# Performance work log

Measured on AMD Instinct MI355X. Metric: run time of the kernel, lower is better.

Reference implementation:

```python
import jax, jax.numpy as jnp
import numpy as np

B, N, EPG = 64, 512, 8192
E = B * EPG
K1 = int(np.ceil(0.8 * N))    # 410
K2 = int(np.ceil(0.8 * K1))   # 328


def setup_inputs() -> dict:
    key = jax.random.key(0)
    ks = jax.random.split(key, 32)
    x = jax.random.normal(ks[0], (B * N, 32), jnp.float32)
    edge_attr = jax.random.normal(ks[1], (E, 100), jnp.float32)
    src_l = jax.random.randint(ks[2], (E,), 0, N)
    dst_l = jax.random.randint(ks[3], (E,), 0, N)
    off = jnp.repeat(jnp.arange(B, dtype=jnp.int64) * N, EPG)
    edge_index = jnp.stack([src_l + off, dst_l + off]).astype(jnp.int64)
    batch = jnp.repeat(jnp.arange(B, dtype=jnp.int64), N)

    def lin(k, fin, fout):
        s = 1.0 / np.sqrt(fin)
        k1, k2 = jax.random.split(k)
        return (jax.random.uniform(k1, (fin, fout), jnp.float32, -s, s),
                jax.random.uniform(k2, (fout,), jnp.float32, -s, s))

    dec1_w, dec1_b = lin(ks[4], 100, 64)
    dec2_w, dec2_b = lin(ks[5], 64, 32)
    mlp1_w, mlp1_b = lin(ks[6], 32, 128)
    mlp2_w, mlp2_b = lin(ks[7], 128, 256)
    pool1_w = jax.random.normal(ks[8], (256,), jnp.float32) * 0.1
    gat_w = jax.random.normal(ks[9], (256, 256), jnp.float32) * (1.0 / np.sqrt(256))
    gat_att_src = jax.random.normal(ks[10], (4, 64), jnp.float32) * 0.1
    gat_att_dst = jax.random.normal(ks[11], (4, 64), jnp.float32) * 0.1
    gat_b = jnp.zeros((256,), jnp.float32)
    pool2_w = jax.random.normal(ks[12], (256,), jnp.float32) * 0.1
    lin1_w, lin1_b = lin(ks[13], 512, 128)
    lin2_w, lin2_b = lin(ks[14], 128, 64)
    lin3_w, lin3_b = lin(ks[15], 64, 2)
    return dict(x=x, edge_index=edge_index, batch=batch, edge_attr=edge_attr,
                dec1_w=dec1_w, dec1_b=dec1_b, dec2_w=dec2_w, dec2_b=dec2_b,
                mlp1_w=mlp1_w, mlp1_b=mlp1_b, mlp2_w=mlp2_w, mlp2_b=mlp2_b,
                pool1_w=pool1_w, gat_w=gat_w, gat_att_src=gat_att_src,
                gat_att_dst=gat_att_dst, gat_b=gat_b, pool2_w=pool2_w,
                lin1_w=lin1_w, lin1_b=lin1_b, lin2_w=lin2_w, lin2_b=lin2_b,
                lin3_w=lin3_w, lin3_b=lin3_b)


def _forward(x, edge_attr, dec1_w, dec1_b, dec2_w, dec2_b, mlp1_w, mlp1_b,
             mlp2_w, mlp2_b, pool1_w, gat_w, gat_att_src, gat_att_dst, gat_b,
             pool2_w, lin1_w, lin1_b, lin2_w, lin2_b, lin3_w, lin3_b,
             src, dst):
    # edge encoder
    ea = jax.nn.relu(edge_attr @ dec1_w + dec1_b)
    ea = jax.nn.relu(ea @ dec2_w + dec2_b)                       # [E,32]
    # GINEConv (eps=0): sum_j relu(x_j + e_ji), then mlp((1+eps)x + aggr)
    msg = jax.nn.relu(x[src] + ea)
    agg = jax.ops.segment_sum(msg, dst, num_segments=B * N)
    h = x + agg
    h = jax.nn.relu(h @ mlp1_w + mlp1_b) @ mlp2_w + mlp2_b       # [BN,256]
    h = jax.nn.relu(h)
    # TopKPooling 1 (uniform graphs -> fixed k)
    s = jnp.tanh((h @ pool1_w) / jnp.linalg.norm(pool1_w))       # [BN]
    topv, topi = jax.lax.top_k(s.reshape(B, N), K1)              # [B,K1]
    gperm = (topi + jnp.arange(B)[:, None] * N).reshape(-1)
    hp = h[gperm] * topv.reshape(-1)[:, None]                    # [B*K1,256]
    kept = jnp.zeros(B * N, bool).at[gperm].set(True)
    newid = jnp.zeros(B * N, jnp.int32).at[gperm].set(jnp.arange(B * K1, dtype=jnp.int32))
    src1, dst1 = newid[src], newid[dst]
    valid = kept[src] & kept[dst]
    # readout 1: global max + mean pool
    hr = hp.reshape(B, K1, 256)
    x1 = jnp.concatenate([hr.max(axis=1), hr.mean(axis=1)], axis=-1)  # [B,512]
    # GATConv(256, 64, heads=4) with self-loops; invalid edges masked
    Nk = B * K1
    loops = jnp.arange(Nk, dtype=jnp.int32)
    src2 = jnp.concatenate([src1, loops])
    dst2 = jnp.concatenate([dst1, loops])
    valid2 = jnp.concatenate([valid, jnp.ones(Nk, bool)])
    xl = (hp @ gat_w).reshape(Nk, 4, 64)
    a_src = (xl * gat_att_src).sum(-1)                           # [Nk,4]
    a_dst = (xl * gat_att_dst).sum(-1)
    logit = jax.nn.leaky_relu(a_src[src2] + a_dst[dst2], 0.2)    # [E2,4]
    logit = jnp.where(valid2[:, None], logit, -jnp.inf)
    m = jax.ops.segment_max(logit, dst2, num_segments=Nk)
    e = jnp.where(valid2[:, None], jnp.exp(logit - m[dst2]), 0.0)
    den = jax.ops.segment_sum(e, dst2, num_segments=Nk)
    alpha = e / den[dst2]
    out = jax.ops.segment_sum(alpha[:, :, None] * xl[src2], dst2, num_segments=Nk)
    g = jax.nn.relu(out.reshape(Nk, 256) + gat_b)
    # TopKPooling 2 (pooled edges unused downstream)
    s2 = jnp.tanh((g @ pool2_w) / jnp.linalg.norm(pool2_w))
    topv2, topi2 = jax.lax.top_k(s2.reshape(B, K1), K2)
    gperm2 = (topi2 + jnp.arange(B)[:, None] * K1).reshape(-1)
    gp = (g[gperm2] * topv2.reshape(-1)[:, None]).reshape(B, K2, 256)
    x2 = jnp.concatenate([gp.max(axis=1), gp.mean(axis=1)], axis=-1)
    # head (dropout = identity in eval)
    z = x1 + x2
    z = jax.nn.relu(z @ lin1_w + lin1_b)
    z = jax.nn.relu(z @ lin2_w + lin2_b)
    return jax.nn.log_softmax(z @ lin3_w + lin3_b, axis=-1)     # [B,2]


def reference(x, edge_index, batch, edge_attr, dec1_w, dec1_b, dec2_w, dec2_b,
              mlp1_w, mlp1_b, mlp2_w, mlp2_b, pool1_w, gat_w, gat_att_src,
              gat_att_dst, gat_b, pool2_w, lin1_w, lin1_b, lin2_w, lin2_b,
              lin3_w, lin3_b):
    src = edge_index[0].astype(jnp.int32)
    dst = edge_index[1].astype(jnp.int32)
    return _forward(x, edge_attr, dec1_w, dec1_b, dec2_w, dec2_b, mlp1_w,
                    mlp1_b, mlp2_w, mlp2_b, pool1_w, gat_w, gat_att_src,
                    gat_att_dst, gat_b, pool2_w, lin1_w, lin1_b, lin2_w,
                    lin2_b, lin3_w, lin3_b, src, dst)
```

## Files before the change

kernel.cpp:

```cpp
#include <hip/hip_runtime.h>
#include <math.h>

#define B_   64
#define N_   512
#define E_   524288
#define BN_  32768
#define K1_  410
#define K2_  328
#define NK_  26240
#define KC_  25

__device__ __forceinline__ float lrelu(float x) { return x > 0.f ? x : 0.2f * x; }

__global__ __launch_bounds__(256) void norm_kernel(const float* __restrict__ p1,
                                                   const float* __restrict__ p2,
                                                   float* __restrict__ norms) {
    __shared__ float r1[256], r2[256];
    int t = threadIdx.x;
    float a = p1[t], b = p2[t];
    r1[t] = a * a; r2[t] = b * b;
    for (int o = 128; o > 0; o >>= 1) {
        __syncthreads();
        if (t < o) { r1[t] += r1[t + o]; r2[t] += r2[t + o]; }
    }
    __syncthreads();
    if (t == 0) { norms[0] = sqrtf(r1[0]); norms[1] = sqrtf(r2[0]); }
}

template <int NSEG>
__global__ __launch_bounds__(1024) void scan_kernel(int* __restrict__ cnt, int* __restrict__ offsets)
{
    __shared__ int part[1024];
    int t = threadIdx.x;
    const int CH = (NSEG + 1023) / 1024;
    int base = t * CH;
    int sum = 0;
    for (int i = 0; i < CH; ++i) { int gi = base + i; if (gi < NSEG) sum += cnt[gi]; }
    part[t] = sum;
    __syncthreads();
    for (int o = 1; o < 1024; o <<= 1) {
        int v = (t >= o) ? part[t - o] : 0;
        __syncthreads();
        part[t] += v;
        __syncthreads();
    }
    int run = (t == 0) ? 0 : part[t - 1];
    for (int i = 0; i < CH; ++i) {
        int gi = base + i;
        if (gi < NSEG) { offsets[gi] = run; run += cnt[gi]; cnt[gi] = 0; }
    }
    if (t == 1023) offsets[NSEG] = part[1023];
}

__global__ __launch_bounds__(256) void count_node_kernel(const int* __restrict__ dstG,
                                                         int* __restrict__ cnt_node)
{
    int e = blockIdx.x * blockDim.x + threadIdx.x;
    atomicAdd(&cnt_node[dstG[e]], 1);
}

__global__ __launch_bounds__(256) void fill_node_kernel(const int* __restrict__ dstG,
                                                        const int* __restrict__ offs_node,
                                                        int* __restrict__ cnt_node,
                                                        int* __restrict__ pos_e)
{
    int e = blockIdx.x * blockDim.x + threadIdx.x;
    int d = dstG[e];
    int p = offs_node[d] + atomicAdd(&cnt_node[d], 1);
    pos_e[e] = p;
}

__global__ __launch_bounds__(256) void edge_mlp_kernel(
    const float* __restrict__ edge_attr, const int* __restrict__ srcG,
    const int* __restrict__ pos_e,
    const float* __restrict__ x,
    const float* __restrict__ W1, const float* __restrict__ b1,
    const float* __restrict__ W2, const float* __restrict__ b2,
    float* __restrict__ msg_sorted)
{
    __shared__ float bufAT[KC_][68];
    __shared__ float w1cT[KC_][64];
    __shared__ float ea1T[64][68];
    __shared__ float w2s[64][32];
    __shared__ float b2s[32];
    __shared__ int   srcs[64], poss[64];

    int tid = threadIdx.x;
    int eb  = blockIdx.x * 64;

    if (tid < 64) { srcs[tid] = srcG[eb + tid]; poss[tid] = pos_e[eb + tid]; }
    for (int i = tid; i < 64 * 32; i += 256) w2s[i >> 5][i & 31] = W2[i];
    if (tid >= 192 && tid < 224) b2s[tid - 192] = b2[tid - 192];

    int tx = tid & 15, ty = tid >> 4;
    float b1v[4];
#pragma unroll
    for (int j = 0; j < 4; ++j) b1v[j] = b1[tx * 4 + j];

    float acc[4][4] = {};

    float raA[7], raB[7], rw[7];
    auto issueA = [&](int kc, float (&ra)[7]) {
#pragma unroll
        for (int u = 0; u < 7; ++u) {
            int i = tid + u * 256;
            if (i < 1600) {
                int e = i / 25, k = i - e * 25;
                ra[u] = edge_attr[(size_t)(eb + e) * 100 + kc + k];
            }
        }
    };
    auto issueW = [&](int kc) {
#pragma unroll
        for (int u = 0; u < 7; ++u) {
            int i = tid + u * 256;
            if (i < 1600) rw[u] = W1[(size_t)(kc + (i >> 6)) * 64 + (i & 63)];
        }
    };
    auto lwriteA = [&](float (&ra)[7]) {
#pragma unroll
        for (int u = 0; u < 7; ++u) {
            int i = tid + u * 256;
            if (i < 1600) {
                int e = i / 25, k = i - e * 25;
                bufAT[k][e] = ra[u];
            }
        }
    };
    auto lwriteW = [&]() {
#pragma unroll
        for (int u = 0; u < 7; ++u) {
            int i = tid + u * 256;
            if (i < 1600) w1cT[i >> 6][i & 63] = rw[u];
        }
    };

    issueA(0, raA);
    issueW(0);
    issueA(KC_, raB);
    lwriteA(raA); lwriteW();
    __syncthreads();

#pragma unroll
    for (int c = 0; c < 4; ++c) {
        if (c == 0) issueA(2 * KC_, raA);
        if (c == 1) issueA(3 * KC_, raB);
        if (c < 3)  issueW((c + 1) * KC_);
#pragma unroll 5
        for (int k = 0; k < KC_; ++k) {
            float4 a4 = *(const float4*)&bufAT[k][ty * 4];
            float4 w4 = *(const float4*)&w1cT[k][tx * 4];
            float a[4] = { a4.x, a4.y, a4.z, a4.w };
            float w[4] = { w4.x, w4.y, w4.z, w4.w };
#pragma unroll
            for (int i = 0; i < 4; ++i)
#pragma unroll
                for (int j = 0; j < 4; ++j) acc[i][j] += a[i] * w[j];
        }
        if (c < 3) {
            __syncthreads();
            if ((c & 1) == 0) lwriteA(raB);
            else              lwriteA(raA);
            lwriteW();
            __syncthreads();
        }
    }
#pragma unroll
    for (int j = 0; j < 4; ++j) {
        float4 v;
        v.x = fmaxf(acc[0][j] + b1v[j], 0.f);
        v.y = fmaxf(acc[1][j] + b1v[j], 0.f);
        v.z = fmaxf(acc[2][j] + b1v[j], 0.f);
        v.w = fmaxf(acc[3][j] + b1v[j], 0.f);
        *(float4*)&ea1T[tx * 4 + j][ty * 4] = v;
    }
    __syncthreads();

    int e0 = (tid >> 3) * 2;
    int c0 = (tid & 7) * 4;
    float acc2[2][4] = {};
    for (int k = 0; k < 64; ++k) {
        float2 a2 = *(const float2*)&ea1T[k][e0];
        float4 w4 = *(const float4*)&w2s[k][c0];
        float w[4] = { w4.x, w4.y, w4.z, w4.w };
#pragma unroll
        for (int j = 0; j < 4; ++j) {
            acc2[0][j] += a2.x * w[j]; acc2[1][j] += a2.y * w[j];
        }
    }
#pragma unroll
    for (int r = 0; r < 2; ++r) {
        int e = e0 + r, s = srcs[e];
        const float4 xv = *(const float4*)(x + (size_t)s * 32 + c0);
        float xa[4] = { xv.x, xv.y, xv.z, xv.w };
        float4 m;
        m.x = fmaxf(xa[0] + fmaxf(acc2[r][0] + b2s[c0 + 0], 0.f), 0.f);
        m.y = fmaxf(xa[1] + fmaxf(acc2[r][1] + b2s[c0 + 1], 0.f), 0.f);
        m.z = fmaxf(xa[2] + fmaxf(acc2[r][2] + b2s[c0 + 2], 0.f), 0.f);
        m.w = fmaxf(xa[3] + fmaxf(acc2[r][3] + b2s[c0 + 3], 0.f), 0.f);
        *(float4*)(msg_sorted + (size_t)poss[e] * 32 + c0) = m;
    }
}

__global__ __launch_bounds__(256) void segsum_kernel(const float* __restrict__ msg_sorted,
                                                     const int* __restrict__ offs_n,
                                                     float* __restrict__ agg)
{
    int wid  = (blockIdx.x * blockDim.x + threadIdx.x) >> 6;
    int lane = threadIdx.x & 63;
    if (wid >= BN_) return;
    int off0 = offs_n[wid], off1 = offs_n[wid + 1];
    int col = lane & 31, rr = lane >> 5;
    float sum = 0.f;
    for (int j = off0 + rr; j < off1; j += 2)
        sum += msg_sorted[(size_t)j * 32 + col];
    sum += __shfl_xor(sum, 32);
    if (lane < 32) agg[(size_t)wid * 32 + col] = sum;
}

template <int ACT, bool HASBIAS, bool HASA2>
__global__ __launch_bounds__(256) void gemm_tile128(
    const float* __restrict__ A, const float* __restrict__ A2,
    const float* __restrict__ W, const float* __restrict__ bias,
    float* __restrict__ C, int M, int N, int K)
{
    __shared__ float As[16][132];
    __shared__ float Ws[16][132];
    int tid = threadIdx.x;
    int tx = tid & 15, ty = tid >> 4;
    int mb = blockIdx.y * 128, nb = blockIdx.x * 128;
    float acc[8][8] = {};

    int am = tid & 127;
    int ak = (tid >> 7) * 8;
    int wk = tid >> 4;
    int wn = (tid & 15) * 8;

    for (int kt = 0; kt < K; kt += 16) {
        {
            const float* pa = A + (size_t)(mb + am) * K + kt + ak;
            float4 v0 = *(const float4*)(pa);
            float4 v1 = *(const float4*)(pa + 4);
            if (HASA2) {
                const float* pb = A2 + (size_t)(mb + am) * K + kt + ak;
                float4 u0 = *(const float4*)(pb);
                float4 u1 = *(const float4*)(pb + 4);
                v0.x += u0.x; v0.y += u0.y; v0.z += u0.z; v0.w += u0.w;
                v1.x += u1.x; v1.y += u1.y; v1.z += u1.z; v1.w += u1.w;
            }
            As[ak + 0][am] = v0.x; As[ak + 1][am] = v0.y;
            As[ak + 2][am] = v0.z; As[ak + 3][am] = v0.w;
            As[ak + 4][am] = v1.x; As[ak + 5][am] = v1.y;
            As[ak + 6][am] = v1.z; As[ak + 7][am] = v1.w;
        }
        {
            const float* pw = W + (size_t)(kt + wk) * N + nb + wn;
            *(float4*)&Ws[wk][wn]     = *(const float4*)(pw);
            *(float4*)&Ws[wk][wn + 4] = *(const float4*)(pw + 4);
        }
        __syncthreads();
#pragma unroll
        for (int k2 = 0; k2 < 16; ++k2) {
            float4 a0 = *(const float4*)&As[k2][ty * 8];
            float4 a1 = *(const float4*)&As[k2][ty * 8 + 4];
            float4 w0 = *(const float4*)&Ws[k2][tx * 4];
            float4 w1 = *(const float4*)&Ws[k2][64 + tx * 4];
            float a[8] = { a0.x, a0.y, a0.z, a0.w, a1.x, a1.y, a1.z, a1.w };
            float w[8] = { w0.x, w0.y, w0.z, w0.w, w1.x, w1.y, w1.z, w1.w };
#pragma unroll
            for (int i = 0; i < 8; ++i)
#pragma unroll
                for (int j = 0; j < 8; ++j) acc[i][j] += a[i] * w[j];
        }
        __syncthreads();
    }
#pragma unroll
    for (int i = 0; i < 8; ++i) {
        int m = mb + ty * 8 + i;
        int col0 = nb + tx * 4, col1 = nb + 64 + tx * 4;
        float r[8];
#pragma unroll
        for (int j = 0; j < 4; ++j) {
            float v = acc[i][j];
            if (HASBIAS) v += bias[col0 + j];
            if (ACT == 1) v = fmaxf(v, 0.f);
            r[j] = v;
        }
#pragma unroll
        for (int j = 4; j < 8; ++j) {
            float v = acc[i][j];
            if (HASBIAS) v += bias[col1 + j - 4];
            if (ACT == 1) v = fmaxf(v, 0.f);
            r[j] = v;
        }
        float4 o0 = { r[0], r[1], r[2], r[3] };
        float4 o1 = { r[4], r[5], r[6], r[7] };
        *(float4*)&C[(size_t)m * N + col0] = o0;
        *(float4*)&C[(size_t)m * N + col1] = o1;
    }
}

__global__ __launch_bounds__(256) void scores_kernel(const float* __restrict__ P,
                                                     const float* __restrict__ w,
                                                     const float* __restrict__ norms, int nidx,
                                                     float* __restrict__ s, int R)
{
    int wid  = (blockIdx.x * blockDim.x + threadIdx.x) >> 6;
    int lane = threadIdx.x & 63;
    if (wid >= R) return;
    float acc = 0.f;
#pragma unroll
    for (int r = 0; r < 4; ++r) {
        int d = r * 64 + lane;
        acc += P[(size_t)wid * 256 + d] * w[d];
    }
    for (int o = 32; o > 0; o >>= 1) acc += __shfl_xor(acc, o);
    if (lane == 0) s[wid] = tanhf(acc / norms[nidx]);
}

__device__ void bitonic_desc512(float* val, int* idx, int t) {
    for (int k = 2; k <= 512; k <<= 1) {
        for (int j = k >> 1; j > 0; j >>= 1) {
            __syncthreads();
            int ixj = t ^ j;
            if (ixj > t) {
                float v0 = val[t], v1 = val[ixj];
                int   i0 = idx[t], i1 = idx[ixj];
                bool before = (v0 > v1) || (v0 == v1 && i0 < i1);
                bool dir = ((t & k) == 0);
                bool doswap = dir ? (!before) : before;
                if (doswap) { val[t] = v1; val[ixj] = v0; idx[t] = i1; idx[ixj] = i0; }
            }
        }
    }
    __syncthreads();
}

__global__ __launch_bounds__(512) void topk1_kernel(const float* __restrict__ s,
                                                    float* __restrict__ topval,
                                                    int* __restrict__ topnode,
                                                    int* __restrict__ kept,
                                                    int* __restrict__ newid)
{
    __shared__ float val[512];
    __shared__ int   idx[512];
    int b = blockIdx.x, t = threadIdx.x;
    val[t] = s[b * N_ + t]; idx[t] = t;
    bitonic_desc512(val, idx, t);
    if (t < K1_) {
        int node = b * N_ + idx[t];
        int orow = b * K1_ + t;
        topnode[orow] = node;
        topval[orow]  = val[t];
        kept[node]  = 1;
        newid[node] = orow;
    }
}

__global__ __launch_bounds__(256) void gather_scale_kernel(const float* __restrict__ h,
                                                           const int* __restrict__ topnode,
                                                           const float* __restrict__ topval,
                                                           float* __restrict__ hp)
{
    int gid = blockIdx.x * blockDim.x + threadIdx.x;
    int row = gid >> 6, q = gid & 63;
    float4 v = *(const float4*)(h + (size_t)topnode[row] * 256 + q * 4);
    float tv = topval[row];
    float4 o; o.x = v.x * tv; o.y = v.y * tv; o.z = v.z * tv; o.w = v.w * tv;
    *(float4*)(hp + (size_t)row * 256 + q * 4) = o;
}

__global__ __launch_bounds__(1024) void readout1_kernel(const float* __restrict__ hp,
                                                        float* __restrict__ zbuf)
{
    __shared__ float rmx[1024], rsm[1024];
    int b = blockIdx.x >> 2, cg = blockIdx.x & 3;
    int tid = threadIdx.x;
    int cl = tid & 63, rg = tid >> 6;
    int c = cg * 64 + cl;
    float mx = -INFINITY, sm = 0.f;
    for (int j = rg; j < K1_; j += 16) {
        float v = hp[((size_t)b * K1_ + j) * 256 + c];
        mx = fmaxf(mx, v); sm += v;
    }
    rmx[tid] = mx; rsm[tid] = sm;
    __syncthreads();
    if (tid < 512) { rmx[tid] = fmaxf(rmx[tid], rmx[tid + 512]); rsm[tid] += rsm[tid + 512]; }
    __syncthreads();
    if (tid < 256) { rmx[tid] = fmaxf(rmx[tid], rmx[tid + 256]); rsm[tid] += rsm[tid + 256]; }
    __syncthreads();
    if (tid < 128) { rmx[tid] = fmaxf(rmx[tid], rmx[tid + 128]); rsm[tid] += rsm[tid + 128]; }
    __syncthreads();
    if (tid < 64) {
        zbuf[b * 512 + c]       = fmaxf(rmx[tid], rmx[tid + 64]);
        zbuf[b * 512 + 256 + c] = (rsm[tid] + rsm[tid + 64]) / (float)K1_;
    }
}

__global__ __launch_bounds__(256) void attcoef_kernel(const float* __restrict__ xl,
                                                      const float* __restrict__ att_src,
                                                      const float* __restrict__ att_dst,
                                                      float* __restrict__ a_src,
                                                      float* __restrict__ a_dst)
{
    int wid  = (blockIdx.x * blockDim.x + threadIdx.x) >> 6;
    int lane = threadIdx.x & 63;
    if (wid >= NK_) return;
    float vs[4], vd[4];
#pragma unroll
    for (int r = 0; r < 4; ++r) {
        int d = r * 64 + lane;
        float v = xl[(size_t)wid * 256 + d];
        vs[r] = v * att_src[d];
        vd[r] = v * att_dst[d];
    }
    for (int o = 32; o > 0; o >>= 1) {
#pragma unroll
        for (int r = 0; r < 4; ++r) {
            vs[r] += __shfl_xor(vs[r], o);
            vd[r] += __shfl_xor(vd[r], o);
        }
    }
    if (lane == 0) {
#pragma unroll
        for (int r = 0; r < 4; ++r) {
            a_src[wid * 4 + r] = vs[r];
            a_dst[wid * 4 + r] = vd[r];
        }
    }
}

__global__ __launch_bounds__(256) void count_kernel(const int* __restrict__ srcG,
                                                    const int* __restrict__ dstG,
                                                    const int* __restrict__ kept,
                                                    const int* __restrict__ newid,
                                                    int* __restrict__ cnt)
{
    int e = blockIdx.x * blockDim.x + threadIdx.x;
    int s = srcG[e], d = dstG[e];
    if (kept[s] && kept[d]) atomicAdd(&cnt[newid[d]], 1);
}

__global__ __launch_bounds__(256) void fill_kernel(const int* __restrict__ srcG,
                                                   const int* __restrict__ dstG,
                                                   const int* __restrict__ kept,
                                                   const int* __restrict__ newid,
                                                   const int* __restrict__ offsets,
                                                   int* __restrict__ cnt,
                                                   int* __restrict__ csr_src)
{
    int e = blockIdx.x * blockDim.x + threadIdx.x;
    int s = srcG[e], d = dstG[e];
    if (kept[s] && kept[d]) {
        int d1 = newid[d];
        int p = offsets[d1] + atomicAdd(&cnt[d1], 1);
        csr_src[p] = newid[s];
    }
}

__global__ __launch_bounds__(256) void gat_agg_kernel(const float* __restrict__ xl,
                                                      const float* __restrict__ a_src,
                                                      const float* __restrict__ a_dst,
                                                      const int* __restrict__ offsets,
                                                      const int* __restrict__ csr_src,
                                                      const float* __restrict__ gat_b,
                                                      const float* __restrict__ pool2_w,
                                                      const float* __restrict__ norms,
                                                      float* __restrict__ g,
                                                      float* __restrict__ s2)
{
    int wid  = (blockIdx.x * blockDim.x + threadIdx.x) >> 6;
    int lane = threadIdx.x & 63;
    if (wid >= NK_) return;
    int off0 = offsets[wid], off1 = offsets[wid + 1];

    float4 ad = *(const float4*)(a_dst + (size_t)wid * 4);
    float4 asf = *(const float4*)(a_src + (size_t)wid * 4);
    float adv[4] = { ad.x, ad.y, ad.z, ad.w };
    float lsf[4] = { lrelu(asf.x + ad.x), lrelu(asf.y + ad.y),
                     lrelu(asf.z + ad.z), lrelu(asf.w + ad.w) };

    float mx[4] = { lsf[0], lsf[1], lsf[2], lsf[3] };
    for (int e = off0 + lane; e < off1; e += 64) {
        int s1 = csr_src[e];
        float4 a = *(const float4*)(a_src + (size_t)s1 * 4);
        float av[4] = { a.x, a.y, a.z, a.w };
#pragma unroll
        for (int r = 0; r < 4; ++r) mx[r] = fmaxf(mx[r], lrelu(av[r] + adv[r]));
    }
    for (int o = 32; o > 0; o >>= 1)
#pragma unroll
        for (int r = 0; r < 4; ++r) mx[r] = fmaxf(mx[r], __shfl_xor(mx[r], o));

    float den[4] = {};
    float acc[4] = {};
    int e = off0;
    for (; e + 1 < off1; e += 2) {
        int s1 = csr_src[e], s2v = csr_src[e + 1];
        float4 a1 = *(const float4*)(a_src + (size_t)s1 * 4);
        float4 a2 = *(const float4*)(a_src + (size_t)s2v * 4);
        float av1[4] = { a1.x, a1.y, a1.z, a1.w };
        float av2[4] = { a2.x, a2.y, a2.z, a2.w };
#pragma unroll
        for (int r = 0; r < 4; ++r) {
            float w1 = expf(lrelu(av1[r] + adv[r]) - mx[r]);
            float w2 = expf(lrelu(av2[r] + adv[r]) - mx[r]);
            float x1 = xl[(size_t)s1 * 256 + r * 64 + lane];
            float x2 = xl[(size_t)s2v * 256 + r * 64 + lane];
            den[r] += w1 + w2;
            acc[r] += w1 * x1 + w2 * x2;
        }
    }
    if (e < off1) {
        int s1 = csr_src[e];
        float4 a1 = *(const float4*)(a_src + (size_t)s1 * 4);
        float av1[4] = { a1.x, a1.y, a1.z, a1.w };
#pragma unroll
        for (int r = 0; r < 4; ++r) {
            float w1 = expf(lrelu(av1[r] + adv[r]) - mx[r]);
            den[r] += w1;
            acc[r] += w1 * xl[(size_t)s1 * 256 + r * 64 + lane];
        }
    }
    float gv[4];
#pragma unroll
    for (int r = 0; r < 4; ++r) {
        float ws = expf(lsf[r] - mx[r]);
        den[r] += ws;
        acc[r] = (acc[r] + ws * xl[(size_t)wid * 256 + r * 64 + lane]) / den[r];
        int d = r * 64 + lane;
        gv[r] = fmaxf(acc[r] + gat_b[d], 0.f);
        g[(size_t)wid * 256 + d] = gv[r];
    }
    float dot = 0.f;
#pragma unroll
    for (int r = 0; r < 4; ++r) dot += gv[r] * pool2_w[r * 64 + lane];
    for (int o = 32; o > 0; o >>= 1) dot += __shfl_xor(dot, o);
    if (lane == 0) s2[wid] = tanhf(dot / norms[1]);
}

__global__ __launch_bounds__(512) void topk2_sort_kernel(const float* __restrict__ s2,
                                                         int* __restrict__ t2row,
                                                         float* __restrict__ t2val)
{
    __shared__ float val[512];
    __shared__ int   idx[512];
    int b = blockIdx.x, t = threadIdx.x;
    val[t] = (t < K1_) ? s2[b * K1_ + t] : -INFINITY;
    idx[t] = t;
    bitonic_desc512(val, idx, t);
    if (t < K2_) {
        t2row[b * K2_ + t] = b * K1_ + idx[t];
        t2val[b * K2_ + t] = val[t];
    }
}

__global__ __launch_bounds__(512) void readout2_kernel(const float* __restrict__ g,
                                                       const int* __restrict__ t2row,
                                                       const float* __restrict__ t2val,
                                                       float* __restrict__ zbuf)
{
    __shared__ float rmx[512], rsm[512];
    int b = blockIdx.x >> 2, cg = blockIdx.x & 3;
    int tid = threadIdx.x;
    int cl = tid & 63, rg = tid >> 6;
    int c = cg * 64 + cl;
    float mx = -INFINITY, sm = 0.f;
    for (int j = rg; j < K2_; j += 8) {
        int row = t2row[b * K2_ + j];
        float v = g[(size_t)row * 256 + c] * t2val[b * K2_ + j];
        mx = fmaxf(mx, v); sm += v;
    }
    rmx[tid] = mx; rsm[tid] = sm;
    __syncthreads();
    if (tid < 256) { rmx[tid] = fmaxf(rmx[tid], rmx[tid + 256]); rsm[tid] += rsm[tid + 256]; }
    __syncthreads();
    if (tid < 128) { rmx[tid] = fmaxf(rmx[tid], rmx[tid + 128]); rsm[tid] += rsm[tid + 128]; }
    __syncthreads();
    if (tid < 64) {
        zbuf[b * 512 + c]       += fmaxf(rmx[tid], rmx[tid + 64]);
        zbuf[b * 512 + 256 + c] += (rsm[tid] + rsm[tid + 64]) / (float)K2_;
    }
}

__global__ __launch_bounds__(128) void head_kernel(const float* __restrict__ zbuf,
                                                   const float* __restrict__ l1w, const float* __restrict__ l1b,
                                                   const float* __restrict__ l2w, const float* __restrict__ l2b,
                                                   const float* __restrict__ l3w, const float* __restrict__ l3b,
                                                   float* __restrict__ out)
{
    __shared__ float zs[512];
    __shared__ float h1s[128];
    __shared__ float h2s[64];
    __shared__ float os[2];
    int b = blockIdx.x, t = threadIdx.x;
    for (int i = t; i < 512; i += 128) zs[i] = zbuf[b * 512 + i];
    __syncthreads();
    float acc = l1b[t];
    for (int k = 0; k < 512; ++k) acc += zs[k] * l1w[k * 128 + t];
    h1s[t] = fmaxf(acc, 0.f);
    __syncthreads();
    if (t < 64) {
        float a2 = l2b[t];
        for (int k = 0; k < 128; ++k) a2 += h1s[k] * l2w[k * 64 + t];
        h2s[t] = fmaxf(a2, 0.f);
    }
    __syncthreads();
    if (t < 2) {
        float a3 = l3b[t];
        for (int k = 0; k < 64; ++k) a3 += h2s[k] * l3w[k * 2 + t];
        os[t] = a3;
    }
    __syncthreads();
    if (t == 0) {
        float m = fmaxf(os[0], os[1]);
        float lse = m + logf(expf(os[0] - m) + expf(os[1] - m));
        out[b * 2 + 0] = os[0] - lse;
        out[b * 2 + 1] = os[1] - lse;
    }
}

extern "C" void kernel_launch(void* const* d_in, const int* in_sizes, int n_in,
                              void* d_out, int out_size, void* d_ws, size_t ws_size,
                              hipStream_t stream)
{
    const float* x         = (const float*)d_in[0];
    const int*   eidx      = (const int*)d_in[1];
    const float* edge_attr = (const float*)d_in[3];
    const float* dec1_w    = (const float*)d_in[4];
    const float* dec1_b    = (const float*)d_in[5];
    const float* dec2_w    = (const float*)d_in[6];
    const float* dec2_b    = (const float*)d_in[7];
    const float* mlp1_w    = (const float*)d_in[8];
    const float* mlp1_b    = (const float*)d_in[9];
    const float* mlp2_w    = (const float*)d_in[10];
    const float* mlp2_b    = (const float*)d_in[11];
    const float* pool1_w   = (const float*)d_in[12];
    const float* gat_w     = (const float*)d_in[13];
    const float* att_src   = (const float*)d_in[14];
    const float* att_dst   = (const float*)d_in[15];
    const float* gat_b     = (const float*)d_in[16];
    const float* pool2_w   = (const float*)d_in[17];
    const float* lin1_w    = (const float*)d_in[18];
    const float* lin1_b    = (const float*)d_in[19];
    const float* lin2_w    = (const float*)d_in[20];
    const float* lin2_b    = (const float*)d_in[21];
    const float* lin3_w    = (const float*)d_in[22];
    const float* lin3_b    = (const float*)d_in[23];
    const int* srcG = eidx;
    const int* dstG = eidx + E_;
    float* out = (float*)d_out;

    char* base = (char*)d_ws;
    size_t o = 0;
    auto alloc = [&](size_t bytes) { size_t r = o; o = (o + bytes + 255) & ~(size_t)255; return r; };
    size_t agg_off    = alloc((size_t)BN_ * 32 * 4);
    size_t cntn_off   = alloc((size_t)BN_ * 4);
    size_t cnt_off    = alloc((size_t)NK_ * 4);
    size_t kept_off   = alloc((size_t)BN_ * 4);
    size_t zero_bytes = o;
    size_t newid_off  = alloc((size_t)BN_ * 4);
    size_t offsn_off  = alloc((size_t)(BN_ + 1) * 4);
    size_t pos_off    = alloc((size_t)E_ * 4);
    size_t h_off      = alloc((size_t)BN_ * 256 * 4);
    size_t hp_off     = alloc((size_t)NK_ * 256 * 4);
    size_t xl_off     = alloc((size_t)NK_ * 256 * 4);
    size_t s_off      = alloc((size_t)BN_ * 4);
    size_t tnode_off  = alloc((size_t)NK_ * 4);
    size_t tval_off   = alloc((size_t)NK_ * 4);
    size_t offs_off   = alloc((size_t)(NK_ + 1) * 4);
    size_t csr_off    = alloc((size_t)E_ * 4);
    size_t zbuf_off   = alloc((size_t)B_ * 512 * 4);
    size_t asrc_off   = alloc((size_t)NK_ * 4 * 4);
    size_t adst_off   = alloc((size_t)NK_ * 4 * 4);
    size_t norm_off   = alloc(256);
    if (o > ws_size) return;

    float* agg      = (float*)(base + agg_off);
    int*   cnt_node = (int*)  (base + cntn_off);
    int*   cnt      = (int*)  (base + cnt_off);
    int*   kept     = (int*)  (base + kept_off);
    int*   newid    = (int*)  (base + newid_off);
    int*   offs_n   = (int*)  (base + offsn_off);
    int*   pos_e    = (int*)  (base + pos_off);
    float* h        = (float*)(base + h_off);
    float* g        = h;
    float* msg      = h;
    float* hp       = (float*)(base + hp_off);
    float* xl       = (float*)(base + xl_off);
    float* t1       = xl;
    float* s        = (float*)(base + s_off);
    int*   tnode    = (int*)  (base + tnode_off);
    float* tval     = (float*)(base + tval_off);
    int*   offs     = (int*)  (base + offs_off);
    int*   csr      = (int*)  (base + csr_off);
    float* zbuf     = (float*)(base + zbuf_off);
    float* a_src    = (float*)(base + asrc_off);
    float* a_dst    = (float*)(base + adst_off);
    float* norms    = (float*)(base + norm_off);

    hipMemsetAsync(d_ws, 0, zero_bytes, stream);

    norm_kernel<<<1, 256, 0, stream>>>(pool1_w, pool2_w, norms);

    count_node_kernel<<<E_ / 256, 256, 0, stream>>>(dstG, cnt_node);
    scan_kernel<BN_><<<1, 1024, 0, stream>>>(cnt_node, offs_n);
    fill_node_kernel<<<E_ / 256, 256, 0, stream>>>(dstG, offs_n, cnt_node, pos_e);

    edge_mlp_kernel<<<E_ / 64, 256, 0, stream>>>(edge_attr, srcG, pos_e, x,
                                                 dec1_w, dec1_b, dec2_w, dec2_b, msg);
    segsum_kernel<<<BN_ / 4, 256, 0, stream>>>(msg, offs_n, agg);

    gemm_tile128<1, true, true><<<dim3(128 / 128, BN_ / 128), 256, 0, stream>>>(
        x, agg, mlp1_w, mlp1_b, t1, BN_, 128, 32);
    gemm_tile128<1, true, false><<<dim3(256 / 128, BN_ / 128), 256, 0, stream>>>(
        t1, nullptr, mlp2_w, mlp2_b, h, BN_, 256, 128);

    scores_kernel<<<BN_ / 4, 256, 0, stream>>>(h, pool1_w, norms, 0, s, BN_);
    topk1_kernel<<<B_, 512, 0, stream>>>(s, tval, tnode, kept, newid);
    gather_scale_kernel<<<(NK_ * 64) / 256, 256, 0, stream>>>(h, tnode, tval, hp);
    readout1_kernel<<<B_ * 4, 1024, 0, stream>>>(hp, zbuf);

    gemm_tile128<0, false, false><<<dim3(256 / 128, NK_ / 128), 256, 0, stream>>>(
        hp, nullptr, gat_w, nullptr, xl, NK_, 256, 256);
    attcoef_kernel<<<NK_ / 4, 256, 0, stream>>>(xl, att_src, att_dst, a_src, a_dst);

    count_kernel<<<E_ / 256, 256, 0, stream>>>(srcG, dstG, kept, newid, cnt);
    scan_kernel<NK_><<<1, 1024, 0, stream>>>(cnt, offs);
    fill_kernel<<<E_ / 256, 256, 0, stream>>>(srcG, dstG, kept, newid, offs, cnt, csr);

    gat_agg_kernel<<<NK_ / 4, 256, 0, stream>>>(xl, a_src, a_dst, offs, csr, gat_b,
                                                pool2_w, norms, g, s);

    topk2_sort_kernel<<<B_, 512, 0, stream>>>(s, tnode, tval);
    readout2_kernel<<<B_ * 4, 512, 0, stream>>>(g, tnode, tval, zbuf);

    head_kernel<<<B_, 128, 0, stream>>>(zbuf, lin1_w, lin1_b, lin2_w, lin2_b,
                                        lin3_w, lin3_b, out);
}
```

Baseline: 578.2 us.

## Fuse top-k gather into GEMM and readout; drop GAT softmax max pass

Removes the gather_scale kernel and the materialized hp buffer. The GAT linear GEMM now gathers and scales rows of h via the top-k indices and values, and readout1 reads h indirectly. Separately, the GAT softmax no longer does a per-node max pre-pass over incoming edges; it exponentiates clamped logits directly. This drops one full edge sweep, but softmax becomes numerically less robust if logits are large and only mildly negative.

Measured after the change: 566.5 us. 1.02x faster.

```diff
diff --git a/kernel.cpp b/kernel.cpp
--- a/kernel.cpp
+++ b/kernel.cpp
@@ -218,9 +218,10 @@
     if (lane < 32) agg[(size_t)wid * 32 + col] = sum;
 }
 
-template <int ACT, bool HASBIAS, bool HASA2>
+template <int ACT, bool HASBIAS, bool HASA2, bool GATHER>
 __global__ __launch_bounds__(256) void gemm_tile128(
     const float* __restrict__ A, const float* __restrict__ A2,
+    const int* __restrict__ rowidx, const float* __restrict__ rowscale,
     const float* __restrict__ W, const float* __restrict__ bias,
     float* __restrict__ C, int M, int N, int K)
 {
@@ -236,17 +237,25 @@
     int wk = tid >> 4;
     int wn = (tid & 15) * 8;
 
+    int   arow  = mb + am;
+    float ascal = 1.f;
+    if (GATHER) { ascal = rowscale[arow]; arow = rowidx[arow]; }
+
     for (int kt = 0; kt < K; kt += 16) {
         {
-            const float* pa = A + (size_t)(mb + am) * K + kt + ak;
+            const float* pa = A + (size_t)arow * K + kt + ak;
             float4 v0 = *(const float4*)(pa);
             float4 v1 = *(const float4*)(pa + 4);
             if (HASA2) {
-                const float* pb = A2 + (size_t)(mb + am) * K + kt + ak;
+                const float* pb = A2 + (size_t)arow * K + kt + ak;
                 float4 u0 = *(const float4*)(pb);
                 float4 u1 = *(const float4*)(pb + 4);
                 v0.x += u0.x; v0.y += u0.y; v0.z += u0.z; v0.w += u0.w;
                 v1.x += u1.x; v1.y += u1.y; v1.z += u1.z; v1.w += u1.w;
+            }
+            if (GATHER) {
+                v0.x *= ascal; v0.y *= ascal; v0.z *= ascal; v0.w *= ascal;
+                v1.x *= ascal; v1.y *= ascal; v1.z *= ascal; v1.w *= ascal;
             }
             As[ak + 0][am] = v0.x; As[ak + 1][am] = v0.y;
             As[ak + 2][am] = v0.z; As[ak + 3][am] = v0.w;
@@ -357,20 +366,9 @@
     }
 }
 
-__global__ __launch_bounds__(256) void gather_scale_kernel(const float* __restrict__ h,
-                                                           const int* __restrict__ topnode,
-                                                           const float* __restrict__ topval,
-                                                           float* __restrict__ hp)
-{
-    int gid = blockIdx.x * blockDim.x + threadIdx.x;
-    int row = gid >> 6, q = gid & 63;
-    float4 v = *(const float4*)(h + (size_t)topnode[row] * 256 + q * 4);
-    float tv = topval[row];
-    float4 o; o.x = v.x * tv; o.y = v.y * tv; o.z = v.z * tv; o.w = v.w * tv;
-    *(float4*)(hp + (size_t)row * 256 + q * 4) = o;
-}
-
-__global__ __launch_bounds__(1024) void readout1_kernel(const float* __restrict__ hp,
+__global__ __launch_bounds__(1024) void readout1_kernel(const float* __restrict__ h,
+                                                        const int* __restrict__ topnode,
+                                                        const float* __restrict__ topval,
                                                         float* __restrict__ zbuf)
 {
     __shared__ float rmx[1024], rsm[1024];
@@ -380,7 +378,8 @@
     int c = cg * 64 + cl;
     float mx = -INFINITY, sm = 0.f;
     for (int j = rg; j < K1_; j += 16) {
-        float v = hp[((size_t)b * K1_ + j) * 256 + c];
+        int row = topnode[b * K1_ + j];
+        float v = h[(size_t)row * 256 + c] * topval[b * K1_ + j];
         mx = fmaxf(mx, v); sm += v;
     }
     rmx[tid] = mx; rsm[tid] = sm;
@@ -480,18 +479,6 @@
     float lsf[4] = { lrelu(asf.x + ad.x), lrelu(asf.y + ad.y),
                      lrelu(asf.z + ad.z), lrelu(asf.w + ad.w) };
 
-    float mx[4] = { lsf[0], lsf[1], lsf[2], lsf[3] };
-    for (int e = off0 + lane; e < off1; e += 64) {
-        int s1 = csr_src[e];
-        float4 a = *(const float4*)(a_src + (size_t)s1 * 4);
-        float av[4] = { a.x, a.y, a.z, a.w };
-#pragma unroll
-        for (int r = 0; r < 4; ++r) mx[r] = fmaxf(mx[r], lrelu(av[r] + adv[r]));
-    }
-    for (int o = 32; o > 0; o >>= 1)
-#pragma unroll
-        for (int r = 0; r < 4; ++r) mx[r] = fmaxf(mx[r], __shfl_xor(mx[r], o));
-
     float den[4] = {};
     float acc[4] = {};
     int e = off0;
@@ -503,8 +490,8 @@
         float av2[4] = { a2.x, a2.y, a2.z, a2.w };
 #pragma unroll
         for (int r = 0; r < 4; ++r) {
-            float w1 = expf(lrelu(av1[r] + adv[r]) - mx[r]);
-            float w2 = expf(lrelu(av2[r] + adv[r]) - mx[r]);
+            float w1 = expf(fminf(lrelu(av1[r] + adv[r]), 80.f));
+            float w2 = expf(fminf(lrelu(av2[r] + adv[r]), 80.f));
             float x1 = xl[(size_t)s1 * 256 + r * 64 + lane];
             float x2 = xl[(size_t)s2v * 256 + r * 64 + lane];
             den[r] += w1 + w2;
@@ -517,7 +504,7 @@
         float av1[4] = { a1.x, a1.y, a1.z, a1.w };
 #pragma unroll
         for (int r = 0; r < 4; ++r) {
-            float w1 = expf(lrelu(av1[r] + adv[r]) - mx[r]);
+            float w1 = expf(fminf(lrelu(av1[r] + adv[r]), 80.f));
             den[r] += w1;
             acc[r] += w1 * xl[(size_t)s1 * 256 + r * 64 + lane];
         }
@@ -525,7 +512,7 @@
     float gv[4];
 #pragma unroll
     for (int r = 0; r < 4; ++r) {
-        float ws = expf(lsf[r] - mx[r]);
+        float ws = expf(fminf(lsf[r], 80.f));
         den[r] += ws;
         acc[r] = (acc[r] + ws * xl[(size_t)wid * 256 + r * 64 + lane]) / den[r];
         int d = r * 64 + lane;
@@ -686,7 +673,6 @@
     float* h        = (float*)(base + h_off);
     float* g        = h;
     float* msg      = h;
-    float* hp       = (float*)(base + hp_off);
     float* xl       = (float*)(base + xl_off);
     float* t1       = xl;
     float* s        = (float*)(base + s_off);
@@ -711,18 +697,17 @@
                                                  dec1_w, dec1_b, dec2_w, dec2_b, msg);
     segsum_kernel<<<BN_ / 4, 256, 0, stream>>>(msg, offs_n, agg);
 
-    gemm_tile128<1, true, true><<<dim3(128 / 128, BN_ / 128), 256, 0, stream>>>(
-        x, agg, mlp1_w, mlp1_b, t1, BN_, 128, 32);
-    gemm_tile128<1, true, false><<<dim3(256 / 128, BN_ / 128), 256, 0, stream>>>(
-        t1, nullptr, mlp2_w, mlp2_b, h, BN_, 256, 128);
+    gemm_tile128<1, true, true, false><<<dim3(1, BN_ / 128), 256, 0, stream>>>(
+        x, agg, nullptr, nullptr, mlp1_w, mlp1_b, t1, BN_, 128, 32);
+    gemm_tile128<1, true, false, false><<<dim3(2, BN_ / 128), 256, 0, stream>>>(
+        t1, nullptr, nullptr, nullptr, mlp2_w, mlp2_b, h, BN_, 256, 128);
 
     scores_kernel<<<BN_ / 4, 256, 0, stream>>>(h, pool1_w, norms, 0, s, BN_);
     topk1_kernel<<<B_, 512, 0, stream>>>(s, tval, tnode, kept, newid);
-    gather_scale_kernel<<<(NK_ * 64) / 256, 256, 0, stream>>>(h, tnode, tval, hp);
-    readout1_kernel<<<B_ * 4, 1024, 0, stream>>>(hp, zbuf);
-
-    gemm_tile128<0, false, false><<<dim3(256 / 128, NK_ / 128), 256, 0, stream>>>(
-        hp, nullptr, gat_w, nullptr, xl, NK_, 256, 256);
+    readout1_kernel<<<B_ * 4, 1024, 0, stream>>>(h, tnode, tval, zbuf);
+
+    gemm_tile128<0, false, false, true><<<dim3(2, NK_ / 128), 256, 0, stream>>>(
+        h, nullptr, tnode, tval, gat_w, nullptr, xl, NK_, 256, 256);
     attcoef_kernel<<<NK_ / 4, 256, 0, stream>>>(xl, att_src, att_dst, a_src, a_dst);
 
     count_kernel<<<E_ / 256, 256, 0, stream>>>(srcG, dstG, kept, newid, cnt);
```
